# Performance work log

Measured on AMD Instinct MI355X. Metric: run time of the kernel, lower is better.

Reference implementation:

```python
import jax, jax.numpy as jnp
import numpy as np
from jax import lax

D = 1024      # dim
E = 2         # expand
DI = D * E    # d_inner = 2048
DS = 16       # d_state
DK = 3        # d_conv (3 so padding=1 preserves seq length)
DTR = 64      # dt_rank = ceil(dim/16)
B = 2
L = 4096


def setup_inputs() -> dict:
    key = jax.random.key(0)
    ks = jax.random.split(key, 8)
    s = 0.02
    return {
        "x": jax.random.normal(ks[0], (B, L, D), jnp.float32),
        "W_in": jax.random.normal(ks[1], (D, 2 * DI), jnp.float32) * s,
        "W_conv": jax.random.normal(ks[2], (DI, 1, DK), jnp.float32) * s,
        "W_xproj": jax.random.normal(ks[3], (DI, DTR + 2 * DS), jnp.float32) * s,
        "W_dt": jax.random.normal(ks[4], (DTR, DI), jnp.float32) * s,
        "b_dt": jax.random.normal(ks[5], (DI,), jnp.float32) * s,
        "W_out": jax.random.normal(ks[6], (DI, D), jnp.float32) * s,
        "ln_g": jnp.ones((DI,), jnp.float32),
        "ln_b": jnp.zeros((DI,), jnp.float32),
    }


def _silu(v):
    return v * jax.nn.sigmoid(v)


def _forward(x, W_in, W_conv, W_xproj, W_dt, b_dt, W_out, ln_g, ln_b):
    # in_proj and gate split
    xz = x @ W_in                                   # (B,L,2*DI)
    xs, z = jnp.split(xz, 2, axis=-1)               # (B,L,DI) each
    # depthwise conv1d (groups = DI), padding preserves L
    xc = lax.conv_general_dilated(
        xs.transpose(0, 2, 1), W_conv, (1,), [(DK // 2, DK // 2)],
        dimension_numbers=("NCH", "OIH", "NCH"), feature_group_count=DI)
    xs = _silu(xc.transpose(0, 2, 1))               # (B,L,DI)
    # x_proj -> dt, B, C
    xp = xs @ W_xproj                               # (B,L,DTR+2*DS)
    dt_lo = xp[..., :DTR]
    Bp = xp[..., DTR:DTR + DS]                      # (B,L,DS)
    Cp = xp[..., DTR + DS:]                         # (B,L,DS)
    dt = jax.nn.softplus(dt_lo @ W_dt + b_dt)       # (B,L,DI)
    # simplified selective scan: scalar decay/input per (b,t)
    dtm = dt.mean(-1)                               # (B,L)
    xm = xs.mean(-1)                                # (B,L)
    decay = jnp.exp(-dtm)                           # (B,L)
    Bx = Bp * xm[..., None]                         # (B,L,DS)

    def step(h, inp):
        d, bx = inp                                 # d:(B,), bx:(B,DS)
        h = h * d[:, None] + bx
        return h, h.sum(-1)                         # emit sum_s h[b,s]

    h0 = jnp.zeros((x.shape[0], DS), x.dtype)
    _, S = lax.scan(step, h0, (decay.T, Bx.transpose(1, 0, 2)))  # S:(L,B)
    y = Cp * S.T[..., None]                         # (B,L,DS): y_t = C_t * sum_s h_t
    y = jnp.tile(y, (1, 1, DI // DS))               # broadcast up to d_inner
    # LayerNorm(d_inner)
    mu = y.mean(-1, keepdims=True)
    var = y.var(-1, keepdims=True)
    y = (y - mu) * lax.rsqrt(var + 1e-5) * ln_g + ln_b
    # gate and out_proj
    y = y * _silu(z)
    return y @ W_out                                # (B,L,D)


def reference(x, W_in, W_conv, W_xproj, W_dt, b_dt, W_out, ln_g, ln_b):
    return _forward(x, W_in, W_conv, W_xproj, W_dt, b_dt, W_out, ln_g, ln_b)
```

## Files before the change

### kernel.cpp

```cpp
#include <hip/hip_runtime.h>
#include <hip/hip_bf16.h>
#include <math.h>
#include <stdint.h>

#define D_    1024
#define DI_   2048
#define DS_   16
#define DTR_  64
#define B_    2
#define L_    4096
#define ROWS_ 8192
#define NXZ_  4096

typedef __attribute__((ext_vector_type(8))) __bf16 bf16x8;
typedef __attribute__((ext_vector_type(4))) float  f32x4;

__device__ __forceinline__ unsigned short f2bf(float f) {
    unsigned u = __float_as_uint(f);
    unsigned r = (u + 0x7fffu + ((u >> 16) & 1u)) >> 16;
    return (unsigned short)r;
}
__device__ __forceinline__ float bf2f(unsigned short h) {
    return __uint_as_float(((unsigned)h) << 16);
}

__device__ __forceinline__ void gload16(const void* gp, void* lp) {
    auto* g1 = (const __attribute__((address_space(1))) unsigned int*)(uintptr_t)gp;
    auto* l3 = (__attribute__((address_space(3))) unsigned int*)(uintptr_t)lp;
    __builtin_amdgcn_global_load_lds(g1, l3, 16, 0, 0);
}

__global__ __launch_bounds__(256) void kcvt(const float* __restrict__ in,
                                            unsigned short* __restrict__ out) {
    const int i = blockIdx.x * 256 + threadIdx.x;
    const float4 v = ((const float4*)in)[i];
    ushort4 o;
    o.x = f2bf(v.x); o.y = f2bf(v.y); o.z = f2bf(v.z); o.w = f2bf(v.w);
    ((ushort4*)out)[i] = o;
}

__global__ __launch_bounds__(256) void ktrans(const float* __restrict__ W,
                                              unsigned short* __restrict__ WT,
                                              int R, int Csrc) {
    __shared__ float tile[32][33];
    const int c0 = blockIdx.x * 32, r0 = blockIdx.y * 32;
    const int tc = threadIdx.x & 31, tr = threadIdx.x >> 5;
#pragma unroll
    for (int i = 0; i < 32; i += 8)
        tile[tr + i][tc] = (c0 + tc < Csrc)
                           ? W[(size_t)(r0 + tr + i) * Csrc + c0 + tc] : 0.f;
    __syncthreads();
#pragma unroll
    for (int i = 0; i < 32; i += 8)
        WT[(size_t)(c0 + tr + i) * R + r0 + tc] = f2bf(tile[tc][tr + i]);
}

template <int K, int NB_SPLIT>
__global__ __launch_bounds__(256, 2) void gemm_bf16(const unsigned short* __restrict__ A,
                                                    const unsigned short* __restrict__ B,
                                                    float* __restrict__ Cf, int ldc,
                                                    unsigned short* __restrict__ Cz) {
    const int t    = threadIdx.x;
    const int wid  = t >> 6, lane = t & 63;
    const int gx  = gridDim.x;
    const int nwg = gx * gridDim.y;
    int lin = blockIdx.y * gx + blockIdx.x;
    lin = (lin & 7) * (nwg >> 3) + (lin >> 3);
    const int bx = lin % gx;
    const int nb = lin / gx;
    const int m0 = bx * 128;
    const int n0 = nb * 128;
    const int wr = wid >> 1, wc = wid & 1;
    __shared__ unsigned short Als[128 * 64];
    __shared__ unsigned short Bls[128 * 64];

    f32x4 acc[4][4];
    const f32x4 z4 = {0.f, 0.f, 0.f, 0.f};
#pragma unroll
    for (int m = 0; m < 4; ++m)
#pragma unroll
        for (int n = 0; n < 4; ++n) acc[m][n] = z4;

    int rowA[4], eoff[4];
#pragma unroll
    for (int i = 0; i < 4; ++i) {
        const int c = wid * 256 + i * 64 + lane;
        rowA[i] = c >> 3;
        eoff[i] = (c & 7) * 8;
    }

    const int ar = wr * 64 + (lane & 15);
    const int br = wc * 64 + (lane & 15);
    const int kq = (lane >> 4) * 8;

    for (int k0 = 0; k0 < K; k0 += 64) {
#pragma unroll
        for (int i = 0; i < 4; ++i) {
            const int dst = (wid * 4 + i) * 1024;
            gload16(A + (size_t)(m0 + rowA[i]) * K + k0 + eoff[i], (char*)Als + dst);
            gload16(B + (size_t)(n0 + rowA[i]) * K + k0 + eoff[i], (char*)Bls + dst);
        }
        __syncthreads();
        bf16x8 af[4][2], bfr[4][2];
#pragma unroll
        for (int m = 0; m < 4; ++m)
#pragma unroll
            for (int kk = 0; kk < 2; ++kk)
                af[m][kk] = *(const bf16x8*)&Als[(ar + m * 16) * 64 + kk * 32 + kq];
#pragma unroll
        for (int n = 0; n < 4; ++n)
#pragma unroll
            for (int kk = 0; kk < 2; ++kk)
                bfr[n][kk] = *(const bf16x8*)&Bls[(br + n * 16) * 64 + kk * 32 + kq];
#pragma unroll
        for (int m = 0; m < 4; ++m)
#pragma unroll
            for (int n = 0; n < 4; ++n)
#pragma unroll
                for (int kk = 0; kk < 2; ++kk)
                    acc[m][n] = __builtin_amdgcn_mfma_f32_16x16x32_bf16(
                        af[m][kk], bfr[n][kk], acc[m][n], 0, 0, 0);
        __syncthreads();
    }

    const int crow = (lane >> 4) * 4, ccol = lane & 15;
    if (nb < NB_SPLIT) {
#pragma unroll
        for (int m = 0; m < 4; ++m)
#pragma unroll
            for (int n = 0; n < 4; ++n)
#pragma unroll
                for (int j = 0; j < 4; ++j)
                    Cf[(size_t)(m0 + wr * 64 + m * 16 + crow + j) * ldc +
                       (n0 + wc * 64 + n * 16 + ccol)] = acc[m][n][j];
    } else {
#pragma unroll
        for (int m = 0; m < 4; ++m)
#pragma unroll
            for (int n = 0; n < 4; ++n)
#pragma unroll
                for (int j = 0; j < 4; ++j)
                    Cz[(size_t)(m0 + wr * 64 + m * 16 + crow + j) * 2048 +
                       (n0 - 2048 + wc * 64 + n * 16 + ccol)] = f2bf(acc[m][n][j]);
    }
}

__global__ __launch_bounds__(256) void k2_conv(const float* __restrict__ xs_raw,
                                               const float* __restrict__ Wcv,
                                               unsigned short* __restrict__ xsb,
                                               float* __restrict__ xm) {
    const int t = threadIdx.x;
    const int wid = t >> 6, lane = t & 63;
    const int row0 = blockIdx.x * 16;
    const int c0 = t * 8;
    __shared__ float wsum[16][4];
    float w0[8], w1[8], w2[8];
#pragma unroll
    for (int j = 0; j < 8; ++j) {
        w0[j] = Wcv[(c0 + j) * 3 + 0];
        w1[j] = Wcv[(c0 + j) * 3 + 1];
        w2[j] = Wcv[(c0 + j) * 3 + 2];
    }
    for (int r = 0; r < 16; ++r) {
        const int row = row0 + r;
        const int l = row & (L_ - 1);
        const float* cur = xs_raw + (size_t)row * DI_ + c0;
        float cv[8], pv[8] = {}, nv[8] = {};
        {
            const float4 a = *(const float4*)cur, b = *(const float4*)(cur + 4);
            cv[0]=a.x; cv[1]=a.y; cv[2]=a.z; cv[3]=a.w;
            cv[4]=b.x; cv[5]=b.y; cv[6]=b.z; cv[7]=b.w;
        }
        if (l > 0) {
            const float4 a = *(const float4*)(cur - DI_), b = *(const float4*)(cur - DI_ + 4);
            pv[0]=a.x; pv[1]=a.y; pv[2]=a.z; pv[3]=a.w;
            pv[4]=b.x; pv[5]=b.y; pv[6]=b.z; pv[7]=b.w;
        }
        if (l < L_ - 1) {
            const float4 a = *(const float4*)(cur + DI_), b = *(const float4*)(cur + DI_ + 4);
            nv[0]=a.x; nv[1]=a.y; nv[2]=a.z; nv[3]=a.w;
            nv[4]=b.x; nv[5]=b.y; nv[6]=b.z; nv[7]=b.w;
        }
        float s8 = 0.f;
        unsigned short o[8];
#pragma unroll
        for (int j = 0; j < 8; ++j) {
            const float v = cv[j] * w1[j] + pv[j] * w0[j] + nv[j] * w2[j];
            const float s = v / (1.f + expf(-v));
            o[j] = f2bf(s);
            s8 += s;
        }
        *(uint4*)(xsb + (size_t)row * DI_ + c0) = *(const uint4*)o;
#pragma unroll
        for (int k = 1; k < 64; k <<= 1) s8 += __shfl_xor(s8, k);
        if (lane == 0) wsum[r][wid] = s8;
    }
    __syncthreads();
    if (t < 16)
        xm[row0 + t] = (wsum[t][0] + wsum[t][1] + wsum[t][2] + wsum[t][3]) * (1.f / (float)DI_);
}

__global__ __launch_bounds__(256, 2) void k3m(const unsigned short* __restrict__ A,
                                              const unsigned short* __restrict__ B,
                                              float* __restrict__ part) {
    const int t = threadIdx.x;
    const int wid = t >> 6, lane = t & 63;
    const int m0 = blockIdx.x * 128;
    const int kc = blockIdx.y;
    const int wr = wid >> 1, wc = wid & 1;
    __shared__ unsigned short Als[128 * 64];
    __shared__ unsigned short Bls[128 * 64];
    f32x4 acc[4][4];
    const f32x4 z4 = {0.f, 0.f, 0.f, 0.f};
#pragma unroll
    for (int m = 0; m < 4; ++m)
#pragma unroll
        for (int n = 0; n < 4; ++n) acc[m][n] = z4;
    int rowA[4], eoff[4];
#pragma unroll
    for (int i = 0; i < 4; ++i) {
        const int c = wid * 256 + i * 64 + lane;
        rowA[i] = c >> 3;
        eoff[i] = (c & 7) * 8;
    }
    const int ar = wr * 64 + (lane & 15);
    const int br = wc * 64 + (lane & 15);
    const int kq = (lane >> 4) * 8;
    const int kbase = kc * 512;
    for (int k0 = kbase; k0 < kbase + 512; k0 += 64) {
#pragma unroll
        for (int i = 0; i < 4; ++i) {
            const int dst = (wid * 4 + i) * 1024;
            gload16(A + (size_t)(m0 + rowA[i]) * DI_ + k0 + eoff[i], (char*)Als + dst);
            gload16(B + (size_t)rowA[i] * DI_ + k0 + eoff[i], (char*)Bls + dst);
        }
        __syncthreads();
        bf16x8 af[4][2], bfr[4][2];
#pragma unroll
        for (int m = 0; m < 4; ++m)
#pragma unroll
            for (int kk = 0; kk < 2; ++kk)
                af[m][kk] = *(const bf16x8*)&Als[(ar + m * 16) * 64 + kk * 32 + kq];
#pragma unroll
        for (int n = 0; n < 4; ++n)
#pragma unroll
            for (int kk = 0; kk < 2; ++kk)
                bfr[n][kk] = *(const bf16x8*)&Bls[(br + n * 16) * 64 + kk * 32 + kq];
#pragma unroll
        for (int m = 0; m < 4; ++m)
#pragma unroll
            for (int n = 0; n < 4; ++n)
#pragma unroll
                for (int kk = 0; kk < 2; ++kk)
                    acc[m][n] = __builtin_amdgcn_mfma_f32_16x16x32_bf16(
                        af[m][kk], bfr[n][kk], acc[m][n], 0, 0, 0);
        __syncthreads();
    }
    const int crow = (lane >> 4) * 4, ccol = lane & 15;
#pragma unroll
    for (int m = 0; m < 4; ++m)
#pragma unroll
        for (int n = 0; n < 4; ++n) {
            const int col = wc * 64 + n * 16 + ccol;
            if (col < 96) {
#pragma unroll
                for (int j = 0; j < 4; ++j)
                    part[((size_t)kc * ROWS_ + m0 + wr * 64 + m * 16 + crow + j) * 96 + col] =
                        acc[m][n][j];
            }
        }
}

__global__ __launch_bounds__(256) void kred(const float* __restrict__ part,
                                            float* __restrict__ xp) {
    const int i = blockIdx.x * 256 + threadIdx.x;
    const size_t stride = (size_t)ROWS_ * 96 / 4;
    const float4* p = (const float4*)part;
    float4 a = p[i], b = p[i + stride], c = p[i + 2 * stride], d = p[i + 3 * stride];
    float4 o;
    o.x = a.x + b.x + c.x + d.x;
    o.y = a.y + b.y + c.y + d.y;
    o.z = a.z + b.z + c.z + d.z;
    o.w = a.w + b.w + c.w + d.w;
    ((float4*)xp)[i] = o;
}

__global__ __launch_bounds__(256) void k4_dt(const float* __restrict__ xp,
                                             const float* __restrict__ Wdt,
                                             const float* __restrict__ bdt,
                                             const float* __restrict__ xm,
                                             float* __restrict__ dec,
                                             float* __restrict__ u) {
    const int r0 = blockIdx.x * 16;
    const int t  = threadIdx.x;
    __shared__ float dlo[16][64];
    __shared__ float Wc[64][65];
    __shared__ float red[16][64];
#pragma unroll
    for (int i = 0; i < 4; ++i) {
        const int e = t + 256 * i;
        const int r = e >> 6, k = e & 63;
        dlo[r][k] = xp[(size_t)(r0 + r) * 96 + k];
    }
    float acc[4] = {};
    const int i_l   = t & 63;
    const int rbase = t >> 6;
    for (int i0 = 0; i0 < DI_; i0 += 64) {
        __syncthreads();
#pragma unroll
        for (int ii = 0; ii < 16; ++ii) {
            const int e = t + 256 * ii;
            const int wk = e >> 6, wi = e & 63;
            Wc[wk][wi] = Wdt[(size_t)wk * DI_ + i0 + wi];
        }
        __syncthreads();
        const float bb2 = bdt[i0 + i_l];
#pragma unroll
        for (int j = 0; j < 4; ++j) {
            const int r = rbase + 4 * j;
            float w = bb2;
#pragma unroll
            for (int k = 0; k < 64; ++k) w += dlo[r][k] * Wc[k][i_l];
            acc[j] += fmaxf(w, 0.f) + log1pf(expf(-fabsf(w)));
        }
    }
    __syncthreads();
#pragma unroll
    for (int j = 0; j < 4; ++j) red[rbase + 4 * j][i_l] = acc[j];
    __syncthreads();
    if (t < 16) {
        float tot = 0.f;
        for (int i = 0; i < 64; ++i) tot += red[t][i];
        const float dtm = tot * (1.f / (float)DI_);
        float sBp = 0.f;
        for (int s = 0; s < DS_; ++s) sBp += xp[(size_t)(r0 + t) * 96 + DTR_ + s];
        dec[r0 + t] = expf(-dtm);
        u[r0 + t]   = xm[r0 + t] * sBp;
    }
}

__global__ __launch_bounds__(256) void k5_scan(const float* __restrict__ dec,
                                               const float* __restrict__ u,
                                               float* __restrict__ S) {
    const int t = threadIdx.x;
    __shared__ float aa[256], hh[256], init[256];
    const int b = t >> 7, c = t & 127;
    const int base = b * L_ + c * 32;
    float a = 1.f, h = 0.f;
    for (int i = 0; i < 32; ++i) {
        const float d = dec[base + i];
        h = h * d + u[base + i];
        a *= d;
    }
    aa[t] = a; hh[t] = h;
    __syncthreads();
    if (t < B_) {
        float run = 0.f;
        for (int cc = 0; cc < 128; ++cc) {
            const int tt = t * 128 + cc;
            init[tt] = run;
            run = hh[tt] + aa[tt] * run;
        }
    }
    __syncthreads();
    h = init[t];
    for (int i = 0; i < 32; ++i) {
        h = h * dec[base + i] + u[base + i];
        S[base + i] = h;
    }
}

__global__ __launch_bounds__(256) void k6_v16(const float* __restrict__ xp,
                                              const float* __restrict__ S,
                                              float* __restrict__ v16) {
    const int row = blockIdx.x * 256 + threadIdx.x;
    const float s = S[row];
    float v[16], mu = 0.f;
#pragma unroll
    for (int i = 0; i < 16; ++i) {
        v[i] = xp[(size_t)row * 96 + DTR_ + DS_ + i] * s;
        mu += v[i];
    }
    mu *= (1.f / 16.f);
    float var = 0.f;
#pragma unroll
    for (int i = 0; i < 16; ++i) {
        const float d = v[i] - mu;
        var += d * d;
    }
    var *= (1.f / 16.f);
    const float rs = rsqrtf(var + 1e-5f);
#pragma unroll
    for (int i = 0; i < 16; ++i) v16[(size_t)row * 16 + i] = (v[i] - mu) * rs;
}

__global__ __launch_bounds__(256) void kA7(const unsigned short* __restrict__ zbf,
                                           const float* __restrict__ v16,
                                           const float* __restrict__ g,
                                           const float* __restrict__ bb,
                                           unsigned short* __restrict__ Abf) {
    const int row = blockIdx.x;
    const int t   = threadIdx.x;
    __shared__ float vrow[16];
    if (t < 16) vrow[t] = v16[row * 16 + t];
    __syncthreads();
    const int i0 = t * 8;
    const uint4 zraw = *(const uint4*)(zbf + (size_t)row * DI_ + i0);
    const unsigned short* zp = (const unsigned short*)&zraw;
    const float4 g0 = *(const float4*)(g + i0),  g1 = *(const float4*)(g + i0 + 4);
    const float4 b0 = *(const float4*)(bb + i0), b1 = *(const float4*)(bb + i0 + 4);
    const float gv[8] = {g0.x, g0.y, g0.z, g0.w, g1.x, g1.y, g1.z, g1.w};
    const float bv[8] = {b0.x, b0.y, b0.z, b0.w, b1.x, b1.y, b1.z, b1.w};
    unsigned short o[8];
#pragma unroll
    for (int j = 0; j < 8; ++j) {
        const int i = i0 + j;
        const float zf = bf2f(zp[j]);
        const float sz = zf / (1.f + expf(-zf));
        o[j] = f2bf((vrow[i & 15] * gv[j] + bv[j]) * sz);
    }
    *(uint4*)(Abf + (size_t)row * DI_ + i0) = *(const uint4*)o;
}

extern "C" void kernel_launch(void* const* d_in, const int* in_sizes, int n_in,
                              void* d_out, int out_size, void* d_ws, size_t ws_size,
                              hipStream_t stream) {
    const float* x    = (const float*)d_in[0];
    const float* Win  = (const float*)d_in[1];
    const float* Wcv  = (const float*)d_in[2];
    const float* Wxp  = (const float*)d_in[3];
    const float* Wdt  = (const float*)d_in[4];
    const float* bdt  = (const float*)d_in[5];
    const float* Wout = (const float*)d_in[6];
    const float* lng  = (const float*)d_in[7];
    const float* lnb  = (const float*)d_in[8];
    float* out = (float*)d_out;

    char* base = (char*)d_ws;
    float*          xs_raw  = (float*)(base + 0);
    unsigned short* Abf     = (unsigned short*)(base + 0);
    unsigned short* zbf     = (unsigned short*)(base + 67108864);
    unsigned short* xsb     = (unsigned short*)(base + 100663296);
    float*          xp_part = (float*)(base + 134217728);
    float*          xp      = (float*)(base + 146800640);
    float*          xm      = (float*)(base + 149946368);
    float*          dec     = (float*)(base + 149979136);
    float*          u       = (float*)(base + 150011904);
    float*          S       = (float*)(base + 150044672);
    float*          v16     = (float*)(base + 150077440);
    unsigned short* xbf     = (unsigned short*)(base + 150601728);
    unsigned short* WoutT   = (unsigned short*)(base + 150601728);
    unsigned short* WinT    = (unsigned short*)(base + 167378944);
    unsigned short* WxpT    = (unsigned short*)(base + 175767552);

    kcvt<<<ROWS_ * D_ / 1024, 256, 0, stream>>>(x, xbf);
    ktrans<<<dim3(NXZ_ / 32, D_ / 32), 256, 0, stream>>>(Win, WinT, D_, NXZ_);
    ktrans<<<dim3(4, DI_ / 32), 256, 0, stream>>>(Wxp, WxpT, DI_, 96);
    gemm_bf16<D_, 16><<<dim3(ROWS_ / 128, NXZ_ / 128), 256, 0, stream>>>(
        xbf, WinT, xs_raw, DI_, zbf);
    ktrans<<<dim3(D_ / 32, DI_ / 32), 256, 0, stream>>>(Wout, WoutT, DI_, D_);
    k2_conv<<<ROWS_ / 16, 256, 0, stream>>>(xs_raw, Wcv, xsb, xm);
    k3m<<<dim3(ROWS_ / 128, 4), 256, 0, stream>>>(xsb, WxpT, xp_part);
    kred<<<ROWS_ * 96 / 4 / 256, 256, 0, stream>>>(xp_part, xp);
    k4_dt<<<ROWS_ / 16, 256, 0, stream>>>(xp, Wdt, bdt, xm, dec, u);
    k5_scan<<<1, 256, 0, stream>>>(dec, u, S);
    k6_v16<<<ROWS_ / 256, 256, 0, stream>>>(xp, S, v16);
    kA7<<<ROWS_, 256, 0, stream>>>(zbf, v16, lng, lnb, Abf);
    gemm_bf16<DI_, 8><<<dim3(ROWS_ / 128, D_ / 128), 256, 0, stream>>>(
        Abf, WoutT, out, D_, (unsigned short*)nullptr);
}
```

Baseline: 449.3 us.

## Move dt projection to bf16 MFMA and store xs in bf16

The dt projection (dt_lo @ W_dt plus softplus and row mean) used to run as a scalar fp32 loop in shared memory. It is now a bf16 MFMA GEMM kernel that reduces softplus sums per row into partial sums, followed by a small reduction kernel. The in_proj GEMM now writes the whole xz output as bf16, so the conv kernel reads half the bytes it read from fp32 before. Launch bounds on the GEMM are raised to 3 waves per SIMD. The cost is bf16 rounding of xs and dt_lo before the conv and the dt projection, which lowers accuracy.

```diff
diff --git a/kernel.cpp b/kernel.cpp
--- a/kernel.cpp
+++ b/kernel.cpp
@@ -55,11 +55,10 @@
         WT[(size_t)(c0 + tr + i) * R + r0 + tc] = f2bf(tile[tc][tr + i]);
 }
 
-template <int K, int NB_SPLIT>
-__global__ __launch_bounds__(256, 2) void gemm_bf16(const unsigned short* __restrict__ A,
+template <int K, bool BF16OUT>
+__global__ __launch_bounds__(256, 3) void gemm_bf16(const unsigned short* __restrict__ A,
                                                     const unsigned short* __restrict__ B,
-                                                    float* __restrict__ Cf, int ldc,
-                                                    unsigned short* __restrict__ Cz) {
+                                                    void* __restrict__ Cp, int ldc) {
     const int t    = threadIdx.x;
     const int wid  = t >> 6, lane = t & 63;
     const int gx  = gridDim.x;
@@ -124,28 +123,20 @@
     }
 
     const int crow = (lane >> 4) * 4, ccol = lane & 15;
-    if (nb < NB_SPLIT) {
-#pragma unroll
-        for (int m = 0; m < 4; ++m)
-#pragma unroll
-            for (int n = 0; n < 4; ++n)
-#pragma unroll
-                for (int j = 0; j < 4; ++j)
-                    Cf[(size_t)(m0 + wr * 64 + m * 16 + crow + j) * ldc +
-                       (n0 + wc * 64 + n * 16 + ccol)] = acc[m][n][j];
-    } else {
-#pragma unroll
-        for (int m = 0; m < 4; ++m)
-#pragma unroll
-            for (int n = 0; n < 4; ++n)
-#pragma unroll
-                for (int j = 0; j < 4; ++j)
-                    Cz[(size_t)(m0 + wr * 64 + m * 16 + crow + j) * 2048 +
-                       (n0 - 2048 + wc * 64 + n * 16 + ccol)] = f2bf(acc[m][n][j]);
-    }
-}
-
-__global__ __launch_bounds__(256) void k2_conv(const float* __restrict__ xs_raw,
+#pragma unroll
+    for (int m = 0; m < 4; ++m)
+#pragma unroll
+        for (int n = 0; n < 4; ++n)
+#pragma unroll
+            for (int j = 0; j < 4; ++j) {
+                const size_t idx = (size_t)(m0 + wr * 64 + m * 16 + crow + j) * ldc +
+                                   (n0 + wc * 64 + n * 16 + ccol);
+                if (BF16OUT) ((unsigned short*)Cp)[idx] = f2bf(acc[m][n][j]);
+                else         ((float*)Cp)[idx] = acc[m][n][j];
+            }
+}
+
+__global__ __launch_bounds__(256) void k2_conv(const unsigned short* __restrict__ xz,
                                                const float* __restrict__ Wcv,
                                                unsigned short* __restrict__ xsb,
                                                float* __restrict__ xm) {
@@ -164,22 +155,25 @@
     for (int r = 0; r < 16; ++r) {
         const int row = row0 + r;
         const int l = row & (L_ - 1);
-        const float* cur = xs_raw + (size_t)row * DI_ + c0;
+        const unsigned short* cur = xz + (size_t)row * NXZ_ + c0;
         float cv[8], pv[8] = {}, nv[8] = {};
         {
-            const float4 a = *(const float4*)cur, b = *(const float4*)(cur + 4);
-            cv[0]=a.x; cv[1]=a.y; cv[2]=a.z; cv[3]=a.w;
-            cv[4]=b.x; cv[5]=b.y; cv[6]=b.z; cv[7]=b.w;
+            const uint4 raw = *(const uint4*)cur;
+            const unsigned short* p = (const unsigned short*)&raw;
+#pragma unroll
+            for (int j = 0; j < 8; ++j) cv[j] = bf2f(p[j]);
         }
         if (l > 0) {
-            const float4 a = *(const float4*)(cur - DI_), b = *(const float4*)(cur - DI_ + 4);
-            pv[0]=a.x; pv[1]=a.y; pv[2]=a.z; pv[3]=a.w;
-            pv[4]=b.x; pv[5]=b.y; pv[6]=b.z; pv[7]=b.w;
+            const uint4 raw = *(const uint4*)(cur - NXZ_);
+            const unsigned short* p = (const unsigned short*)&raw;
+#pragma unroll
+            for (int j = 0; j < 8; ++j) pv[j] = bf2f(p[j]);
         }
         if (l < L_ - 1) {
-            const float4 a = *(const float4*)(cur + DI_), b = *(const float4*)(cur + DI_ + 4);
-            nv[0]=a.x; nv[1]=a.y; nv[2]=a.z; nv[3]=a.w;
-            nv[4]=b.x; nv[5]=b.y; nv[6]=b.z; nv[7]=b.w;
+            const uint4 raw = *(const uint4*)(cur + NXZ_);
+            const unsigned short* p = (const unsigned short*)&raw;
+#pragma unroll
+            for (int j = 0; j < 8; ++j) nv[j] = bf2f(p[j]);
         }
         float s8 = 0.f;
         unsigned short o[8];
@@ -272,7 +266,8 @@
 }
 
 __global__ __launch_bounds__(256) void kred(const float* __restrict__ part,
-                                            float* __restrict__ xp) {
+                                            float* __restrict__ xp,
+                                            unsigned short* __restrict__ dtlo) {
     const int i = blockIdx.x * 256 + threadIdx.x;
     const size_t stride = (size_t)ROWS_ * 96 / 4;
     const float4* p = (const float4*)part;
@@ -283,60 +278,104 @@
     o.z = a.z + b.z + c.z + d.z;
     o.w = a.w + b.w + c.w + d.w;
     ((float4*)xp)[i] = o;
-}
-
-__global__ __launch_bounds__(256) void k4_dt(const float* __restrict__ xp,
-                                             const float* __restrict__ Wdt,
-                                             const float* __restrict__ bdt,
-                                             const float* __restrict__ xm,
-                                             float* __restrict__ dec,
-                                             float* __restrict__ u) {
-    const int r0 = blockIdx.x * 16;
-    const int t  = threadIdx.x;
-    __shared__ float dlo[16][64];
-    __shared__ float Wc[64][65];
-    __shared__ float red[16][64];
+    const int c4 = i % 24, row = i / 24;
+    if (c4 < 16) {
+        ushort4 h;
+        h.x = f2bf(o.x); h.y = f2bf(o.y); h.z = f2bf(o.z); h.w = f2bf(o.w);
+        *(ushort4*)(dtlo + (size_t)row * 64 + c4 * 4) = h;
+    }
+}
+
+__global__ __launch_bounds__(256, 2) void k4m(const unsigned short* __restrict__ A,
+                                              const unsigned short* __restrict__ B,
+                                              const float* __restrict__ bdt,
+                                              float* __restrict__ psum) {
+    const int t = threadIdx.x;
+    const int wid = t >> 6, lane = t & 63;
+    const int m0 = blockIdx.x * 128;
+    const int nb = blockIdx.y;
+    const int wr = wid >> 1, wc = wid & 1;
+    __shared__ unsigned short Als[128 * 64];
+    __shared__ unsigned short Bls[128 * 64];
+    __shared__ float srow[128][2];
+    f32x4 acc[4][4];
+    const f32x4 z4 = {0.f, 0.f, 0.f, 0.f};
+#pragma unroll
+    for (int m = 0; m < 4; ++m)
+#pragma unroll
+        for (int n = 0; n < 4; ++n) acc[m][n] = z4;
 #pragma unroll
     for (int i = 0; i < 4; ++i) {
-        const int e = t + 256 * i;
-        const int r = e >> 6, k = e & 63;
-        dlo[r][k] = xp[(size_t)(r0 + r) * 96 + k];
-    }
-    float acc[4] = {};
-    const int i_l   = t & 63;
-    const int rbase = t >> 6;
-    for (int i0 = 0; i0 < DI_; i0 += 64) {
-        __syncthreads();
-#pragma unroll
-        for (int ii = 0; ii < 16; ++ii) {
-            const int e = t + 256 * ii;
-            const int wk = e >> 6, wi = e & 63;
-            Wc[wk][wi] = Wdt[(size_t)wk * DI_ + i0 + wi];
-        }
-        __syncthreads();
-        const float bb2 = bdt[i0 + i_l];
+        const int c = wid * 256 + i * 64 + lane;
+        const int row = c >> 3, eo = (c & 7) * 8;
+        const int dst = (wid * 4 + i) * 1024;
+        gload16(A + (size_t)(m0 + row) * 64 + eo, (char*)Als + dst);
+        gload16(B + (size_t)(nb * 128 + row) * 64 + eo, (char*)Bls + dst);
+    }
+    __syncthreads();
+    const int ar = wr * 64 + (lane & 15);
+    const int br = wc * 64 + (lane & 15);
+    const int kq = (lane >> 4) * 8;
+    const int ccol = lane & 15;
+    {
+        bf16x8 af[4][2], bfr[4][2];
+#pragma unroll
+        for (int m = 0; m < 4; ++m)
+#pragma unroll
+            for (int kk = 0; kk < 2; ++kk)
+                af[m][kk] = *(const bf16x8*)&Als[(ar + m * 16) * 64 + kk * 32 + kq];
+#pragma unroll
+        for (int n = 0; n < 4; ++n)
+#pragma unroll
+            for (int kk = 0; kk < 2; ++kk)
+                bfr[n][kk] = *(const bf16x8*)&Bls[(br + n * 16) * 64 + kk * 32 + kq];
+#pragma unroll
+        for (int m = 0; m < 4; ++m)
+#pragma unroll
+            for (int n = 0; n < 4; ++n)
+#pragma unroll
+                for (int kk = 0; kk < 2; ++kk)
+                    acc[m][n] = __builtin_amdgcn_mfma_f32_16x16x32_bf16(
+                        af[m][kk], bfr[n][kk], acc[m][n], 0, 0, 0);
+    }
+    float bcol[4];
+#pragma unroll
+    for (int n = 0; n < 4; ++n) bcol[n] = bdt[nb * 128 + wc * 64 + n * 16 + ccol];
+#pragma unroll
+    for (int m = 0; m < 4; ++m)
 #pragma unroll
         for (int j = 0; j < 4; ++j) {
-            const int r = rbase + 4 * j;
-            float w = bb2;
-#pragma unroll
-            for (int k = 0; k < 64; ++k) w += dlo[r][k] * Wc[k][i_l];
-            acc[j] += fmaxf(w, 0.f) + log1pf(expf(-fabsf(w)));
-        }
-    }
-    __syncthreads();
-#pragma unroll
-    for (int j = 0; j < 4; ++j) red[rbase + 4 * j][i_l] = acc[j];
-    __syncthreads();
-    if (t < 16) {
-        float tot = 0.f;
-        for (int i = 0; i < 64; ++i) tot += red[t][i];
-        const float dtm = tot * (1.f / (float)DI_);
-        float sBp = 0.f;
-        for (int s = 0; s < DS_; ++s) sBp += xp[(size_t)(r0 + t) * 96 + DTR_ + s];
-        dec[r0 + t] = expf(-dtm);
-        u[r0 + t]   = xm[r0 + t] * sBp;
-    }
+            float s = 0.f;
+#pragma unroll
+            for (int n = 0; n < 4; ++n) {
+                const float w = acc[m][n][j] + bcol[n];
+                s += fmaxf(w, 0.f) + log1pf(expf(-fabsf(w)));
+            }
+#pragma unroll
+            for (int mask = 1; mask < 16; mask <<= 1) s += __shfl_xor(s, mask);
+            if (ccol == 0)
+                srow[wr * 64 + m * 16 + (lane >> 4) * 4 + j][wc] = s;
+        }
+    __syncthreads();
+    if (t < 128)
+        psum[(size_t)nb * ROWS_ + m0 + t] = srow[t][0] + srow[t][1];
+}
+
+__global__ __launch_bounds__(256) void k4r(const float* __restrict__ psum,
+                                           const float* __restrict__ xp,
+                                           const float* __restrict__ xm,
+                                           float* __restrict__ dec,
+                                           float* __restrict__ u) {
+    const int row = blockIdx.x * 256 + threadIdx.x;
+    float tot = 0.f;
+#pragma unroll
+    for (int j = 0; j < 16; ++j) tot += psum[(size_t)j * ROWS_ + row];
+    const float dtm = tot * (1.f / (float)DI_);
+    float sBp = 0.f;
+#pragma unroll
+    for (int s = 0; s < DS_; ++s) sBp += xp[(size_t)row * 96 + DTR_ + s];
+    dec[row] = expf(-dtm);
+    u[row]   = xm[row] * sBp;
 }
 
 __global__ __launch_bounds__(256) void k5_scan(const float* __restrict__ dec,
@@ -394,7 +433,7 @@
     for (int i = 0; i < 16; ++i) v16[(size_t)row * 16 + i] = (v[i] - mu) * rs;
 }
 
-__global__ __launch_bounds__(256) void kA7(const unsigned short* __restrict__ zbf,
+__global__ __launch_bounds__(256) void kA7(const unsigned short* __restrict__ xz,
                                            const float* __restrict__ v16,
                                            const float* __restrict__ g,
                                            const float* __restrict__ bb,
@@ -405,7 +444,7 @@
     if (t < 16) vrow[t] = v16[row * 16 + t];
     __syncthreads();
     const int i0 = t * 8;
-    const uint4 zraw = *(const uint4*)(zbf + (size_t)row * DI_ + i0);
+    const uint4 zraw = *(const uint4*)(xz + (size_t)row * NXZ_ + 2048 + i0);
     const unsigned short* zp = (const unsigned short*)&zraw;
     const float4 g0 = *(const float4*)(g + i0),  g1 = *(const float4*)(g + i0 + 4);
     const float4 b0 = *(const float4*)(bb + i0), b1 = *(const float4*)(bb + i0 + 4);
@@ -437,35 +476,39 @@
     float* out = (float*)d_out;
 
     char* base = (char*)d_ws;
-    float*          xs_raw  = (float*)(base + 0);
-    unsigned short* Abf     = (unsigned short*)(base + 0);
-    unsigned short* zbf     = (unsigned short*)(base + 67108864);
-    unsigned short* xsb     = (unsigned short*)(base + 100663296);
-    float*          xp_part = (float*)(base + 134217728);
-    float*          xp      = (float*)(base + 146800640);
-    float*          xm      = (float*)(base + 149946368);
-    float*          dec     = (float*)(base + 149979136);
-    float*          u       = (float*)(base + 150011904);
-    float*          S       = (float*)(base + 150044672);
-    float*          v16     = (float*)(base + 150077440);
-    unsigned short* xbf     = (unsigned short*)(base + 150601728);
-    unsigned short* WoutT   = (unsigned short*)(base + 150601728);
-    unsigned short* WinT    = (unsigned short*)(base + 167378944);
-    unsigned short* WxpT    = (unsigned short*)(base + 175767552);
+    unsigned short* xz_bf   = (unsigned short*)(base + 0);
+    unsigned short* xsb     = (unsigned short*)(base + 67108864);
+    unsigned short* xbf     = (unsigned short*)(base + 100663296);
+    unsigned short* Abf     = (unsigned short*)(base + 100663296);
+    unsigned short* WoutT   = (unsigned short*)(base + 134217728);
+    unsigned short* WinT    = (unsigned short*)(base + 138412032);
+    unsigned short* WxpT    = (unsigned short*)(base + 146800640);
+    unsigned short* WdtT    = (unsigned short*)(base + 147324928);
+    float*          xp_part = (float*)(base + 147587072);
+    float*          xp      = (float*)(base + 160169984);
+    unsigned short* dtlo    = (unsigned short*)(base + 163315712);
+    float*          psum    = (float*)(base + 164364288);
+    float*          xm      = (float*)(base + 164888576);
+    float*          dec     = (float*)(base + 164921344);
+    float*          u       = (float*)(base + 164954112);
+    float*          S       = (float*)(base + 164986880);
+    float*          v16     = (float*)(base + 165019648);
 
     kcvt<<<ROWS_ * D_ / 1024, 256, 0, stream>>>(x, xbf);
     ktrans<<<dim3(NXZ_ / 32, D_ / 32), 256, 0, stream>>>(Win, WinT, D_, NXZ_);
     ktrans<<<dim3(4, DI_ / 32), 256, 0, stream>>>(Wxp, WxpT, DI_, 96);
-    gemm_bf16<D_, 16><<<dim3(ROWS_ / 128, NXZ_ / 128), 256, 0, stream>>>(
-        xbf, WinT, xs_raw, DI_, zbf);
+    ktrans<<<dim3(DI_ / 32, DTR_ / 32), 256, 0, stream>>>(Wdt, WdtT, DTR_, DI_);
+    gemm_bf16<D_, true><<<dim3(ROWS_ / 128, NXZ_ / 128), 256, 0, stream>>>(
+        xbf, WinT, xz_bf, NXZ_);
     ktrans<<<dim3(D_ / 32, DI_ / 32), 256, 0, stream>>>(Wout, WoutT, DI_, D_);
-    k2_conv<<<ROWS_ / 16, 256, 0, stream>>>(xs_raw, Wcv, xsb, xm);
+    k2_conv<<<ROWS_ / 16, 256, 0, stream>>>(xz_bf, Wcv, xsb, xm);
     k3m<<<dim3(ROWS_ / 128, 4), 256, 0, stream>>>(xsb, WxpT, xp_part);
-    kred<<<ROWS_ * 96 / 4 / 256, 256, 0, stream>>>(xp_part, xp);
-    k4_dt<<<ROWS_ / 16, 256, 0, stream>>>(xp, Wdt, bdt, xm, dec, u);
+    kred<<<ROWS_ * 96 / 4 / 256, 256, 0, stream>>>(xp_part, xp, dtlo);
+    k4m<<<dim3(ROWS_ / 128, DI_ / 128), 256, 0, stream>>>(dtlo, WdtT, bdt, psum);
+    k4r<<<ROWS_ / 256, 256, 0, stream>>>(psum, xp, xm, dec, u);
     k5_scan<<<1, 256, 0, stream>>>(dec, u, S);
     k6_v16<<<ROWS_ / 256, 256, 0, stream>>>(xp, S, v16);
-    kA7<<<ROWS_, 256, 0, stream>>>(zbf, v16, lng, lnb, Abf);
-    gemm_bf16<DI_, 8><<<dim3(ROWS_ / 128, D_ / 128), 256, 0, stream>>>(
-        Abf, WoutT, out, D_, (unsigned short*)nullptr);
-}
+    kA7<<<ROWS_, 256, 0, stream>>>(xz_bf, v16, lng, lnb, Abf);
+    gemm_bf16<DI_, false><<<dim3(ROWS_ / 128, D_ / 128), 256, 0, stream>>>(
+        Abf, WoutT, out, D_);
+}
```

New measurement: 387.4 us. 1.16x faster.
